# Kernel tuning notes

Hardware: AMD Instinct MI355X
Metric: run time of the kernel (lower is better)

## Reference

```python
import jax, jax.numpy as jnp
import numpy as np
import math

N = 30000
E = 600000
IN_DIM = 256
HID = 64
EMB = 64
HEADS = 4
EPS = 1e-5


def _glorot(key, shape):
    fan_in, fan_out = shape[0], shape[1]
    lim = math.sqrt(6.0 / (fan_in + fan_out))
    return jax.random.uniform(key, shape, jnp.float32, -lim, lim)


def setup_inputs() -> dict:
    key = jax.random.key(0)
    ks = jax.random.split(key, 24)
    inp = {
        "x": jax.random.normal(ks[0], (N, IN_DIM), jnp.float32),
        "edge_index": jax.random.randint(ks[1], (2, E), 0, N, jnp.int64),
    }
    # layer 1: in=IN_DIM, out per head=HID, heads=HEADS -> width HID*HEADS
    w1 = HID * HEADS
    inp.update({
        "w1q": _glorot(ks[2], (IN_DIM, w1)), "b1q": jnp.zeros((w1,), jnp.float32),
        "w1k": _glorot(ks[3], (IN_DIM, w1)), "b1k": jnp.zeros((w1,), jnp.float32),
        "w1v": _glorot(ks[4], (IN_DIM, w1)), "b1v": jnp.zeros((w1,), jnp.float32),
        "w1s": _glorot(ks[5], (IN_DIM, w1)), "b1s": jnp.zeros((w1,), jnp.float32),
        "g1": jnp.ones((w1,), jnp.float32), "be1": jnp.zeros((w1,), jnp.float32),
    })
    # layer 2: in=HID*HEADS, out per head=EMB -> width EMB*HEADS
    w2 = EMB * HEADS
    inp.update({
        "w2q": _glorot(ks[6], (w1, w2)), "b2q": jnp.zeros((w2,), jnp.float32),
        "w2k": _glorot(ks[7], (w1, w2)), "b2k": jnp.zeros((w2,), jnp.float32),
        "w2v": _glorot(ks[8], (w1, w2)), "b2v": jnp.zeros((w2,), jnp.float32),
        "w2s": _glorot(ks[9], (w1, w2)), "b2s": jnp.zeros((w2,), jnp.float32),
        "g2": jnp.ones((w2,), jnp.float32), "be2": jnp.zeros((w2,), jnp.float32),
    })
    return inp


def transformer_conv(x, edge_index, wq, bq, wk, bk, wv, bv, ws, bs, heads, out_ch):
    n = x.shape[0]
    q = (x @ wq + bq).reshape(n, heads, out_ch)
    k = (x @ wk + bk).reshape(n, heads, out_ch)
    v = (x @ wv + bv).reshape(n, heads, out_ch)
    src, dst = edge_index[0], edge_index[1]
    # per-edge gather: [E, H, C]
    qi, kj, vj = q[dst], k[src], v[src]
    alpha = jnp.sum(qi * kj, axis=-1) / math.sqrt(out_ch)  # [E, H]
    # segment softmax over incoming edges of each target node
    amax = jax.lax.stop_gradient(jax.ops.segment_max(alpha, dst, num_segments=n))
    ex = jnp.exp(alpha - amax[dst])
    denom = jax.ops.segment_sum(ex, dst, num_segments=n)
    alpha = ex / denom[dst]
    # scatter-add weighted values back to targets
    out = jax.ops.segment_sum(vj * alpha[..., None], dst, num_segments=n)
    out = out.reshape(n, heads * out_ch)
    return out + x @ ws + bs  # root/skip connection


def batch_norm(x, gamma, beta):
    mean = jnp.mean(x, axis=0)
    var = jnp.mean(jnp.square(x - mean), axis=0)  # biased, training-mode BN
    return (x - mean) * jax.lax.rsqrt(var + EPS) * gamma + beta


def leaky_relu(x):
    return jnp.where(x >= 0, x, 0.1 * x)


def reference(x, edge_index, w1q, b1q, w1k, b1k, w1v, b1v, w1s, b1s, g1, be1,
              w2q, b2q, w2k, b2k, w2v, b2v, w2s, b2s, g2, be2):
    h = transformer_conv(x, edge_index, w1q, b1q, w1k, b1k, w1v, b1v, w1s, b1s, HEADS, HID)
    h = leaky_relu(batch_norm(h, g1, be1))
    h = transformer_conv(h, edge_index, w2q, b2q, w2k, b2k, w2v, b2v, w2s, b2s, HEADS, EMB)
    h = leaky_relu(batch_norm(h, g2, be2))
    return h
```

## Files before the change

### kernel.cpp

```cpp
#include <hip/hip_runtime.h>
#include <math.h>

#define NODES 30000
#define EDGES 600000
#define QKVS_W 1024
#define OUT_W 256
#define BN_EPS 1e-5f

typedef _Float16 f16x8 __attribute__((ext_vector_type(8)));
typedef _Float16 half2t __attribute__((ext_vector_type(2)));
typedef __attribute__((ext_vector_type(4))) float f32x4;

__device__ __forceinline__ unsigned short f2h(float f) {
    union { _Float16 h; unsigned short u; } v;
    v.h = (_Float16)f;
    return v.u;
}
__device__ __forceinline__ float h2f(unsigned short u) {
    union { unsigned short u; _Float16 h; } v; v.u = u;
    return (float)v.h;
}
__device__ __forceinline__ half2t u2h2(unsigned int u) {
    union { unsigned int u; half2t h; } v; v.u = u;
    return v.h;
}

__device__ __forceinline__ float fdot2(half2t a, half2t b, float c) {
#if __has_builtin(__builtin_amdgcn_fdot2)
    return __builtin_amdgcn_fdot2(a, b, c, false);
#else
    return fmaf((float)a.x, (float)b.x, fmaf((float)a.y, (float)b.y, c));
#endif
}

template<int CTRL>
__device__ __forceinline__ float dpp_xor_add(float x) {
    int xi = __builtin_bit_cast(int, x);
    int yi = __builtin_amdgcn_mov_dpp(xi, CTRL, 0xF, 0xF, true);
    return x + __builtin_bit_cast(float, yi);
}

typedef const __attribute__((address_space(1))) void* gas_p;
typedef __attribute__((address_space(3))) void* las_p;
__device__ __forceinline__ void gload_lds16(const void* g, void* l) {
    __builtin_amdgcn_global_load_lds((gas_p)g, (las_p)l, 16, 0, 0);
}


__global__ __launch_bounds__(256) void k_count(const int* __restrict__ ei, int* __restrict__ deg) {
    int e = blockIdx.x * 256 + threadIdx.x;
    if (e < EDGES) atomicAdd(&deg[ei[EDGES + e]], 1);
}

__global__ __launch_bounds__(256) void k_blocksum(const int* __restrict__ deg, int* __restrict__ bsum) {
    __shared__ int sh[256];
    int i = blockIdx.x * 256 + threadIdx.x;
    sh[threadIdx.x] = (i < NODES) ? deg[i] : 0;
    __syncthreads();
    for (int off = 128; off > 0; off >>= 1) {
        if (threadIdx.x < off) sh[threadIdx.x] += sh[threadIdx.x + off];
        __syncthreads();
    }
    if (threadIdx.x == 0) bsum[blockIdx.x] = sh[0];
}

__global__ __launch_bounds__(128) void k_scanb(const int* __restrict__ bsum, int* __restrict__ bbase, int nb) {
    __shared__ int sh[128];
    int t = threadIdx.x;
    int v = (t < nb) ? bsum[t] : 0;
    sh[t] = v;
    __syncthreads();
    for (int off = 1; off < 128; off <<= 1) {
        int add = (t >= off) ? sh[t - off] : 0;
        __syncthreads();
        sh[t] += add;
        __syncthreads();
    }
    if (t < nb) bbase[t] = sh[t] - v;
}

__global__ __launch_bounds__(256) void k_localscan(const int* __restrict__ deg, const int* __restrict__ bbase,
                                                   int* __restrict__ rowptr, int* __restrict__ cursor) {
    __shared__ int sh[256];
    int i = blockIdx.x * 256 + threadIdx.x;
    int v = (i < NODES) ? deg[i] : 0;
    sh[threadIdx.x] = v;
    __syncthreads();
    for (int off = 1; off < 256; off <<= 1) {
        int add = (threadIdx.x >= off) ? sh[threadIdx.x - off] : 0;
        __syncthreads();
        sh[threadIdx.x] += add;
        __syncthreads();
    }
    if (i < NODES) {
        int p = bbase[blockIdx.x] + sh[threadIdx.x] - v;
        rowptr[i] = p;
        cursor[i] = p;
    }
}

__global__ __launch_bounds__(256) void k_fill(const int* __restrict__ ei, int* __restrict__ cursor,
                                              int* __restrict__ csr_src) {
    int e = blockIdx.x * 256 + threadIdx.x;
    if (e < EDGES) {
        int s = ei[e];
        int d = ei[EDGES + e];
        int slot = atomicAdd(&cursor[d], 1);
        csr_src[slot] = s;
    }
}


__global__ __launch_bounds__(256) void k_castA(const float* __restrict__ in, unsigned short* __restrict__ out, int n8) {
    int i = blockIdx.x * 256 + threadIdx.x;
    if (i >= n8) return;
    const float4* p = (const float4*)(in + (size_t)i * 8);
    float4 v0 = p[0], v1 = p[1];
    ushort4 o0, o1;
    o0.x = f2h(v0.x); o0.y = f2h(v0.y); o0.z = f2h(v0.z); o0.w = f2h(v0.w);
    o1.x = f2h(v1.x); o1.y = f2h(v1.y); o1.z = f2h(v1.z); o1.w = f2h(v1.w);
    ushort4* q = (ushort4*)(out + (size_t)i * 8);
    q[0] = o0; q[1] = o1;
}

__global__ __launch_bounds__(256) void k_castW2(
    const float* __restrict__ Wa0, const float* __restrict__ Wa1,
    const float* __restrict__ Wa2, const float* __restrict__ Wa3,
    const float* __restrict__ Ba0, const float* __restrict__ Ba1,
    const float* __restrict__ Ba2, const float* __restrict__ Ba3,
    const float* __restrict__ Wb0, const float* __restrict__ Wb1,
    const float* __restrict__ Wb2, const float* __restrict__ Wb3,
    const float* __restrict__ Bb0, const float* __restrict__ Bb1,
    const float* __restrict__ Bb2, const float* __restrict__ Bb3,
    unsigned short* __restrict__ Wt1, float* __restrict__ bf1,
    unsigned short* __restrict__ Wt2, float* __restrict__ bf2)
{
    int nn0 = blockIdx.x;
    int layer = nn0 >> 10;
    int n = nn0 & 1023;
    int k = threadIdx.x;
    int wsel = n >> 8, nc = n & 255;
    const float* W; const float* Bv;
    if (layer == 0) {
        W  = (wsel == 0) ? Wa0 : (wsel == 1) ? Wa1 : (wsel == 2) ? Wa2 : Wa3;
        Bv = (wsel == 0) ? Ba0 : (wsel == 1) ? Ba1 : (wsel == 2) ? Ba2 : Ba3;
    } else {
        W  = (wsel == 0) ? Wb0 : (wsel == 1) ? Wb1 : (wsel == 2) ? Wb2 : Wb3;
        Bv = (wsel == 0) ? Bb0 : (wsel == 1) ? Bb1 : (wsel == 2) ? Bb2 : Bb3;
    }
    unsigned short* Wt = (layer == 0) ? Wt1 : Wt2;
    float* bfused = (layer == 0) ? bf1 : bf2;
    Wt[(size_t)n * 256 + k] = f2h(W[(size_t)k * 256 + nc]);
    if (k == 0) bfused[n] = Bv[nc];
}


#define CS 136

__global__ __launch_bounds__(256) void k_gemm_f16(
    const unsigned short* __restrict__ A,
    const unsigned short* __restrict__ Wt,
    const float* __restrict__ bias,
    unsigned short* __restrict__ C, int M)
{
    __shared__ unsigned short sbuf[128 * CS];
    unsigned short* As = sbuf;
    unsigned short* Bs = sbuf + 8192;
    int tid = threadIdx.x;
    int lane = tid & 63;
    int wave = tid >> 6;
    int wm = wave & 1, wn = wave >> 1;
    int row0 = blockIdx.x * 128;
    int n0 = blockIdx.y * 128;

    f32x4 acc[4][4] = {};

    for (int k0 = 0; k0 < 256; k0 += 64) {
        #pragma unroll
        for (int w = 0; w < 4; w++) {
            int c = w * 256 + tid;
            int row = c >> 3;
            int cole = (c & 7) * 8;
            int ar = row0 + row; if (ar >= M) ar = M - 1;
            gload_lds16(&A[(size_t)ar * 256 + k0 + cole], &As[w * 2048 + tid * 8]);
            gload_lds16(&Wt[(size_t)(n0 + row) * 256 + k0 + cole], &Bs[w * 2048 + tid * 8]);
        }
        __syncthreads();
        int rsel = lane & 15;
        int kq = (lane >> 4) * 8;
        #pragma unroll
        for (int kh = 0; kh < 2; kh++) {
            f16x8 af[4], bfr[4];
            #pragma unroll
            for (int t = 0; t < 4; t++) {
                af[t]  = *reinterpret_cast<const f16x8*>(&As[(wm * 64 + t * 16 + rsel) * 64 + kh * 32 + kq]);
                bfr[t] = *reinterpret_cast<const f16x8*>(&Bs[(wn * 64 + t * 16 + rsel) * 64 + kh * 32 + kq]);
            }
            #pragma unroll
            for (int mt = 0; mt < 4; mt++)
                #pragma unroll
                for (int nt = 0; nt < 4; nt++)
                    acc[mt][nt] = __builtin_amdgcn_mfma_f32_16x16x32_f16(af[mt], bfr[nt], acc[mt][nt], 0, 0, 0);
        }
        __syncthreads();
    }

    int crow = (lane >> 4) * 4;
    int ccol = lane & 15;
    #pragma unroll
    for (int mt = 0; mt < 4; mt++) {
        int lrow = wm * 64 + mt * 16 + crow;
        #pragma unroll
        for (int nt = 0; nt < 4; nt++) {
            int lcol = wn * 64 + nt * 16 + ccol;
            float bv = bias[n0 + lcol];
            #pragma unroll
            for (int r = 0; r < 4; r++)
                sbuf[(lrow + r) * CS + lcol] = f2h(acc[mt][nt][r] + bv);
        }
    }
    __syncthreads();
    int chunk = tid & 15;
    int rbase = tid >> 4;
    #pragma unroll
    for (int g = 0; g < 8; g++) {
        int row_l = g * 16 + rbase;
        int gr = row0 + row_l;
        if (gr < M) {
            uint4 val = *(const uint4*)&sbuf[row_l * CS + chunk * 8];
            *(uint4*)&C[(size_t)gr * QKVS_W + n0 + chunk * 8] = val;
        }
    }
}


__global__ __launch_bounds__(256) void k_attn_f16(const unsigned short* __restrict__ qkvs,
                                                  const int* __restrict__ rowptr,
                                                  const int* __restrict__ deg,
                                                  const int* __restrict__ csr_src,
                                                  float* __restrict__ out)
{
    int wave = threadIdx.x >> 6;
    int lane = threadIdx.x & 63;
    int node = blockIdx.x * 4 + wave;
    if (node >= NODES) return;
    int half = lane >> 5;
    int lh = lane & 31;

    const unsigned short* qrow = qkvs + (size_t)node * QKVS_W;
    uint4 qv = *(const uint4*)&qrow[lh * 8];

    int start = rowptr[node];
    int cnt = deg[node];

    float m = -INFINITY, L = 0.f;
    float acc[8] = {0.f, 0.f, 0.f, 0.f, 0.f, 0.f, 0.f, 0.f};

    if (cnt > 0) {
        int clast = cnt - 1;
        #define CPOS(p) (start + (((2 * (p) + half) > clast) ? clast : (2 * (p) + half)))
        int i0  = csr_src[CPOS(0)];
        int i1  = csr_src[CPOS(1)];
        int ixA = csr_src[CPOS(2)];
        int ixB = csr_src[CPOS(3)];
        uint4 kA, vA, kB, vB;
        {
            const unsigned short* p = qkvs + (size_t)i0 * QKVS_W + lh * 8;
            kA = *(const uint4*)(p + 256);
            vA = *(const uint4*)(p + 512);
        }
        {
            const unsigned short* p = qkvs + (size_t)i1 * QKVS_W + lh * 8;
            kB = *(const uint4*)(p + 256);
            vB = *(const uint4*)(p + 512);
        }
        int npairs = (cnt + 1) >> 1;
        for (int i = 0; i < npairs; i += 2) {
            {
                const unsigned short* pA = qkvs + (size_t)ixA * QKVS_W + lh * 8;
                ixA = csr_src[CPOS(i + 4)];
                float d  = fdot2(u2h2(qv.x), u2h2(kA.x), 0.f);
                d        = fdot2(u2h2(qv.y), u2h2(kA.y), d);
                float d2 = fdot2(u2h2(qv.z), u2h2(kA.z), 0.f);
                d2       = fdot2(u2h2(qv.w), u2h2(kA.w), d2);
                d += d2;
                kA = *(const uint4*)(pA + 256);
                d = dpp_xor_add<0xB1>(d);
                d = dpp_xor_add<0x4E>(d);
                d = dpp_xor_add<0x141>(d);
                float al = d * 0.125f;
                bool valid = (2 * i + half) < cnt;
                if (valid) {
                    if (__any(al > m + 8.f)) {
                        float nm = fmaxf(m, al);
                        float sc = __expf(m - nm);
                        L *= sc;
                        #pragma unroll
                        for (int t = 0; t < 8; t++) acc[t] *= sc;
                        m = nm;
                    }
                    float p = __expf(al - m);
                    L += p;
                    half2t vh0 = u2h2(vA.x), vh1 = u2h2(vA.y);
                    half2t vh2 = u2h2(vA.z), vh3 = u2h2(vA.w);
                    acc[0] = fmaf((float)vh0.x, p, acc[0]);
                    acc[1] = fmaf((float)vh0.y, p, acc[1]);
                    acc[2] = fmaf((float)vh1.x, p, acc[2]);
                    acc[3] = fmaf((float)vh1.y, p, acc[3]);
                    acc[4] = fmaf((float)vh2.x, p, acc[4]);
                    acc[5] = fmaf((float)vh2.y, p, acc[5]);
                    acc[6] = fmaf((float)vh3.x, p, acc[6]);
                    acc[7] = fmaf((float)vh3.y, p, acc[7]);
                }
                vA = *(const uint4*)(pA + 512);
            }
            {
                const unsigned short* pB = qkvs + (size_t)ixB * QKVS_W + lh * 8;
                ixB = csr_src[CPOS(i + 5)];
                float d  = fdot2(u2h2(qv.x), u2h2(kB.x), 0.f);
                d        = fdot2(u2h2(qv.y), u2h2(kB.y), d);
                float d2 = fdot2(u2h2(qv.z), u2h2(kB.z), 0.f);
                d2       = fdot2(u2h2(qv.w), u2h2(kB.w), d2);
                d += d2;
                kB = *(const uint4*)(pB + 256);
                d = dpp_xor_add<0xB1>(d);
                d = dpp_xor_add<0x4E>(d);
                d = dpp_xor_add<0x141>(d);
                float al = d * 0.125f;
                bool valid = (2 * (i + 1) + half) < cnt;
                if (valid) {
                    if (__any(al > m + 8.f)) {
                        float nm = fmaxf(m, al);
                        float sc = __expf(m - nm);
                        L *= sc;
                        #pragma unroll
                        for (int t = 0; t < 8; t++) acc[t] *= sc;
                        m = nm;
                    }
                    float p = __expf(al - m);
                    L += p;
                    half2t vh0 = u2h2(vB.x), vh1 = u2h2(vB.y);
                    half2t vh2 = u2h2(vB.z), vh3 = u2h2(vB.w);
                    acc[0] = fmaf((float)vh0.x, p, acc[0]);
                    acc[1] = fmaf((float)vh0.y, p, acc[1]);
                    acc[2] = fmaf((float)vh1.x, p, acc[2]);
                    acc[3] = fmaf((float)vh1.y, p, acc[3]);
                    acc[4] = fmaf((float)vh2.x, p, acc[4]);
                    acc[5] = fmaf((float)vh2.y, p, acc[5]);
                    acc[6] = fmaf((float)vh3.x, p, acc[6]);
                    acc[7] = fmaf((float)vh3.y, p, acc[7]);
                }
                vB = *(const uint4*)(pB + 512);
            }
        }
        #undef CPOS
    }

    float mo = __shfl_xor(m, 32, 64);
    float Lo = __shfl_xor(L, 32, 64);
    float nm = fmaxf(m, mo);
    float scs = (L  > 0.f) ? __expf(m  - nm) : 0.f;
    float sco = (Lo > 0.f) ? __expf(mo - nm) : 0.f;
    float Lt = fmaf(L, scs, Lo * sco);
    float inv = (Lt > 0.f) ? 1.f / Lt : 0.f;
    float t0 = fmaf(acc[0], scs, __shfl_xor(acc[0], 32, 64) * sco);
    float t1 = fmaf(acc[1], scs, __shfl_xor(acc[1], 32, 64) * sco);
    float t2 = fmaf(acc[2], scs, __shfl_xor(acc[2], 32, 64) * sco);
    float t3 = fmaf(acc[3], scs, __shfl_xor(acc[3], 32, 64) * sco);
    float t4 = fmaf(acc[4], scs, __shfl_xor(acc[4], 32, 64) * sco);
    float t5 = fmaf(acc[5], scs, __shfl_xor(acc[5], 32, 64) * sco);
    float t6 = fmaf(acc[6], scs, __shfl_xor(acc[6], 32, 64) * sco);
    float t7 = fmaf(acc[7], scs, __shfl_xor(acc[7], 32, 64) * sco);
    float w0 = half ? t4 : t0;
    float w1 = half ? t5 : t1;
    float w2 = half ? t6 : t2;
    float w3 = half ? t7 : t3;
    ushort4 sv = *(const ushort4*)&qrow[768 + lh * 8 + half * 4];
    float4 o;
    o.x = fmaf(w0, inv, h2f(sv.x));
    o.y = fmaf(w1, inv, h2f(sv.y));
    o.z = fmaf(w2, inv, h2f(sv.z));
    o.w = fmaf(w3, inv, h2f(sv.w));
    *(float4*)&out[(size_t)node * OUT_W + lh * 8 + half * 4] = o;
}


__global__ __launch_bounds__(256) void k_bnstats(const float* __restrict__ h,
                                                 float* __restrict__ sum, float* __restrict__ sumsq) {
    int col = threadIdx.x;
    int r0 = blockIdx.x * 64;
    int r1 = min(r0 + 64, NODES);
    float s = 0.f, s2 = 0.f;
    for (int r = r0; r < r1; r++) {
        float v = h[(size_t)r * OUT_W + col];
        s += v; s2 += v * v;
    }
    atomicAdd(&sum[col], s);
    atomicAdd(&sumsq[col], s2);
}

__device__ __forceinline__ float4 bn_scale4(const float* sum, const float* sumsq,
                                            const float* g, const float* be,
                                            int col, float4* shift) {
    float4 s  = *(const float4*)&sum[col];
    float4 s2 = *(const float4*)&sumsq[col];
    float4 gv = *(const float4*)&g[col];
    float4 bv = *(const float4*)&be[col];
    const float invN = 1.0f / NODES;
    float4 sc, sh;
    float mean, var;
    mean = s.x * invN; var = fmaxf(s2.x * invN - mean * mean, 0.f);
    sc.x = gv.x * rsqrtf(var + BN_EPS); sh.x = bv.x - mean * sc.x;
    mean = s.y * invN; var = fmaxf(s2.y * invN - mean * mean, 0.f);
    sc.y = gv.y * rsqrtf(var + BN_EPS); sh.y = bv.y - mean * sc.y;
    mean = s.z * invN; var = fmaxf(s2.z * invN - mean * mean, 0.f);
    sc.z = gv.z * rsqrtf(var + BN_EPS); sh.z = bv.z - mean * sc.z;
    mean = s.w * invN; var = fmaxf(s2.w * invN - mean * mean, 0.f);
    sc.w = gv.w * rsqrtf(var + BN_EPS); sh.w = bv.w - mean * sc.w;
    *shift = sh;
    return sc;
}

__global__ __launch_bounds__(256) void k_bnapply_f16(const float* __restrict__ h,
                                                     const float* __restrict__ sum,
                                                     const float* __restrict__ sumsq,
                                                     const float* __restrict__ g,
                                                     const float* __restrict__ be,
                                                     unsigned short* __restrict__ out) {
    int idx = blockIdx.x * 256 + threadIdx.x;
    int base = idx * 4;
    int col = base & (OUT_W - 1);
    float4 sh;
    float4 sc = bn_scale4(sum, sumsq, g, be, col, &sh);
    float4 v = *(const float4*)&h[base];
    float4 o;
    o.x = v.x * sc.x + sh.x; o.x = (o.x >= 0.f) ? o.x : 0.1f * o.x;
    o.y = v.y * sc.y + sh.y; o.y = (o.y >= 0.f) ? o.y : 0.1f * o.y;
    o.z = v.z * sc.z + sh.z; o.z = (o.z >= 0.f) ? o.z : 0.1f * o.z;
    o.w = v.w * sc.w + sh.w; o.w = (o.w >= 0.f) ? o.w : 0.1f * o.w;
    ushort4 u; u.x = f2h(o.x); u.y = f2h(o.y); u.z = f2h(o.z); u.w = f2h(o.w);
    *(ushort4*)&out[base] = u;
}

__global__ __launch_bounds__(256) void k_bnapply(const float* __restrict__ h,
                                                 const float* __restrict__ sum,
                                                 const float* __restrict__ sumsq,
                                                 const float* __restrict__ g,
                                                 const float* __restrict__ be,
                                                 float* __restrict__ out) {
    int idx = blockIdx.x * 256 + threadIdx.x;
    int base = idx * 4;
    int col = base & (OUT_W - 1);
    float4 sh;
    float4 sc = bn_scale4(sum, sumsq, g, be, col, &sh);
    float4 v = *(const float4*)&h[base];
    float4 o;
    o.x = v.x * sc.x + sh.x; o.x = (o.x >= 0.f) ? o.x : 0.1f * o.x;
    o.y = v.y * sc.y + sh.y; o.y = (o.y >= 0.f) ? o.y : 0.1f * o.y;
    o.z = v.z * sc.z + sh.z; o.z = (o.z >= 0.f) ? o.z : 0.1f * o.z;
    o.w = v.w * sc.w + sh.w; o.w = (o.w >= 0.f) ? o.w : 0.1f * o.w;
    *(float4*)&out[base] = o;
}


extern "C" void kernel_launch(void* const* d_in, const int* in_sizes, int n_in,
                              void* d_out, int out_size, void* d_ws, size_t ws_size,
                              hipStream_t stream) {
    const float* x  = (const float*)d_in[0];
    const int*   ei = (const int*)d_in[1];
    const float* w1[4] = {(const float*)d_in[2], (const float*)d_in[4], (const float*)d_in[6], (const float*)d_in[8]};
    const float* b1[4] = {(const float*)d_in[3], (const float*)d_in[5], (const float*)d_in[7], (const float*)d_in[9]};
    const float* g1  = (const float*)d_in[10];
    const float* be1 = (const float*)d_in[11];
    const float* w2[4] = {(const float*)d_in[12], (const float*)d_in[14], (const float*)d_in[16], (const float*)d_in[18]};
    const float* b2[4] = {(const float*)d_in[13], (const float*)d_in[15], (const float*)d_in[17], (const float*)d_in[19]};
    const float* g2  = (const float*)d_in[20];
    const float* be2 = (const float*)d_in[21];

    char* ws = (char*)d_ws;
    unsigned short* qkvsb  = (unsigned short*)(ws);
    float*          h1     = (float*)(ws + 61440000);
    unsigned short* abuf   = (unsigned short*)(ws + 92160000);
    unsigned short* wt1    = (unsigned short*)(ws + 107520000);
    unsigned short* wt2    = (unsigned short*)(ws + 108044288);
    float*          b1f    = (float*)(ws + 108568576);
    float*          b2f    = (float*)(ws + 108572672);
    int*            deg    = (int*)  (ws + 108576768);
    int*            rowptr = (int*)  (ws + 108696768);
    int*            cursor = (int*)  (ws + 108816768);
    int*            csr    = (int*)  (ws + 108936768);
    int*            bsum   = (int*)  (ws + 111336768);
    int*            bbase  = (int*)  (ws + 111337280);
    float*          sum1   = (float*)(ws + 111337792);
    float*          sq1    = (float*)(ws + 111338816);
    float*          sum2   = (float*)(ws + 111339840);
    float*          sq2    = (float*)(ws + 111340864);

    hipMemsetAsync(deg, 0, NODES * sizeof(int), stream);
    hipMemsetAsync(sum1, 0, 4096, stream);

    const int EB = (EDGES + 255) / 256;
    const int NB = (NODES + 255) / 256;

    k_castA<<<(NODES * 256 / 8 + 255) / 256, 256, 0, stream>>>(x, abuf, NODES * 256 / 8);
    k_castW2<<<2048, 256, 0, stream>>>(w1[0], w1[1], w1[2], w1[3], b1[0], b1[1], b1[2], b1[3],
                                       w2[0], w2[1], w2[2], w2[3], b2[0], b2[1], b2[2], b2[3],
                                       wt1, b1f, wt2, b2f);

    k_count    <<<EB, 256, 0, stream>>>(ei, deg);
    k_blocksum <<<NB, 256, 0, stream>>>(deg, bsum);
    k_scanb    <<<1, 128, 0, stream>>>(bsum, bbase, NB);
    k_localscan<<<NB, 256, 0, stream>>>(deg, bbase, rowptr, cursor);
    k_fill     <<<EB, 256, 0, stream>>>(ei, cursor, csr);

    dim3 ggrid((NODES + 127) / 128, 8);
    const int ANB = NODES / 4;
    const int APB = (NODES * OUT_W / 4) / 256;
    const int SNB = (NODES + 63) / 64;

    k_gemm_f16   <<<ggrid, 256, 0, stream>>>(abuf, wt1, b1f, qkvsb, NODES);
    k_attn_f16   <<<ANB, 256, 0, stream>>>(qkvsb, rowptr, deg, csr, h1);
    k_bnstats    <<<SNB, 256, 0, stream>>>(h1, sum1, sq1);
    k_bnapply_f16<<<APB, 256, 0, stream>>>(h1, sum1, sq1, g1, be1, abuf);

    k_gemm_f16   <<<ggrid, 256, 0, stream>>>(abuf, wt2, b2f, qkvsb, NODES);
    k_attn_f16   <<<ANB, 256, 0, stream>>>(qkvsb, rowptr, deg, csr, h1);
    k_bnstats    <<<SNB, 256, 0, stream>>>(h1, sum2, sq2);
    k_bnapply    <<<APB, 256, 0, stream>>>(h1, sum2, sq2, g2, be2, (float*)d_out);
}
```

Measured before the change: 510.8 us.

## Split QKVS buffer into separate Q/S, K fp16, and FP8 V arrays

The GEMM epilogue now writes Q and skip into one 512-wide fp16 buffer, K into its own dense 256-wide fp16 buffer, and V as FP8 (e4m3) into a 256-byte-per-row buffer. The attention kernel gathers K and V from these compact arrays and decodes V with the packed fp8-to-f32 conversion. This cuts the bytes moved by the random per-edge gathers and packs the gathered rows more tightly for better cache use. The cost is lower V precision, which may push results outside tolerance, plus extra encode and decode work.

```diff
diff --git a/kernel.cpp b/kernel.cpp
--- a/kernel.cpp
+++ b/kernel.cpp
@@ -3,12 +3,15 @@
 
 #define NODES 30000
 #define EDGES 600000
-#define QKVS_W 1024
+#define QS_W 512
+#define K_W 256
+#define KV_W 256
 #define OUT_W 256
 #define BN_EPS 1e-5f
 
 typedef _Float16 f16x8 __attribute__((ext_vector_type(8)));
 typedef _Float16 half2t __attribute__((ext_vector_type(2)));
+typedef float f32x2 __attribute__((ext_vector_type(2)));
 typedef __attribute__((ext_vector_type(4))) float f32x4;
 
 __device__ __forceinline__ unsigned short f2h(float f) {
@@ -31,6 +34,54 @@
 #else
     return fmaf((float)a.x, (float)b.x, fmaf((float)a.y, (float)b.y, c));
 #endif
+}
+
+
+__device__ __forceinline__ void dec8(uint2 w, float* f) {
+#if __has_builtin(__builtin_amdgcn_cvt_pk_f32_fp8)
+    f32x2 a = __builtin_amdgcn_cvt_pk_f32_fp8((int)w.x, false);
+    f32x2 b = __builtin_amdgcn_cvt_pk_f32_fp8((int)w.x, true);
+    f32x2 c = __builtin_amdgcn_cvt_pk_f32_fp8((int)w.y, false);
+    f32x2 d = __builtin_amdgcn_cvt_pk_f32_fp8((int)w.y, true);
+    f[0] = a.x; f[1] = a.y; f[2] = b.x; f[3] = b.y;
+    f[4] = c.x; f[5] = c.y; f[6] = d.x; f[7] = d.y;
+#else
+    #pragma unroll
+    for (int j = 0; j < 8; j++) {
+        unsigned int byte = ((j < 4 ? w.x : w.y) >> ((j & 3) * 8)) & 0xFF;
+        unsigned short h = (unsigned short)(((byte & 0x80u) << 8) | ((byte & 0x7Fu) << 7));
+        f[j] = h2f(h) * 256.0f;
+    }
+#endif
+}
+
+__device__ __forceinline__ uint2 enc8(uint4 w) {
+    float f[8];
+    f[0] = h2f((unsigned short)(w.x & 0xffff)); f[1] = h2f((unsigned short)(w.x >> 16));
+    f[2] = h2f((unsigned short)(w.y & 0xffff)); f[3] = h2f((unsigned short)(w.y >> 16));
+    f[4] = h2f((unsigned short)(w.z & 0xffff)); f[5] = h2f((unsigned short)(w.z >> 16));
+    f[6] = h2f((unsigned short)(w.w & 0xffff)); f[7] = h2f((unsigned short)(w.w >> 16));
+    uint2 r;
+#if __has_builtin(__builtin_amdgcn_cvt_pk_fp8_f32)
+    int lo = 0, hi = 0;
+    lo = __builtin_amdgcn_cvt_pk_fp8_f32(f[0], f[1], lo, false);
+    lo = __builtin_amdgcn_cvt_pk_fp8_f32(f[2], f[3], lo, true);
+    hi = __builtin_amdgcn_cvt_pk_fp8_f32(f[4], f[5], hi, false);
+    hi = __builtin_amdgcn_cvt_pk_fp8_f32(f[6], f[7], hi, true);
+    r.x = (unsigned)lo; r.y = (unsigned)hi;
+#else
+    unsigned b[8];
+    #pragma unroll
+    for (int j = 0; j < 8; j++) {
+        unsigned short hb = f2h(f[j] * 0.00390625f);
+        unsigned m = hb & 0x7fffu;
+        unsigned rr = m + 0x3Fu + ((m >> 7) & 1u);
+        b[j] = ((hb >> 8) & 0x80u) | ((rr >> 7) & 0x7Fu);
+    }
+    r.x = b[0] | (b[1] << 8) | (b[2] << 16) | (b[3] << 24);
+    r.y = b[4] | (b[5] << 8) | (b[6] << 16) | (b[7] << 24);
+#endif
+    return r;
 }
 
 template<int CTRL>
@@ -161,7 +212,9 @@
     const unsigned short* __restrict__ A,
     const unsigned short* __restrict__ Wt,
     const float* __restrict__ bias,
-    unsigned short* __restrict__ C, int M)
+    unsigned short* __restrict__ QS,
+    unsigned short* __restrict__ K16,
+    unsigned char* __restrict__ V8, int M)
 {
     __shared__ unsigned short sbuf[128 * CS];
     unsigned short* As = sbuf;
@@ -222,19 +275,47 @@
     __syncthreads();
     int chunk = tid & 15;
     int rbase = tid >> 4;
-    #pragma unroll
-    for (int g = 0; g < 8; g++) {
-        int row_l = g * 16 + rbase;
-        int gr = row0 + row_l;
-        if (gr < M) {
-            uint4 val = *(const uint4*)&sbuf[row_l * CS + chunk * 8];
-            *(uint4*)&C[(size_t)gr * QKVS_W + n0 + chunk * 8] = val;
-        }
-    }
-}
-
-
-__global__ __launch_bounds__(256) void k_attn_f16(const unsigned short* __restrict__ qkvs,
+    if (n0 < 256 || n0 >= 768) {
+        int cbase = (n0 < 256) ? n0 : (n0 - 512);
+        #pragma unroll
+        for (int g = 0; g < 8; g++) {
+            int row_l = g * 16 + rbase;
+            int gr = row0 + row_l;
+            if (gr < M) {
+                uint4 val = *(const uint4*)&sbuf[row_l * CS + chunk * 8];
+                *(uint4*)&QS[(size_t)gr * QS_W + cbase + chunk * 8] = val;
+            }
+        }
+    } else if (n0 < 512) {
+        int cbase = n0 - 256;
+        #pragma unroll
+        for (int g = 0; g < 8; g++) {
+            int row_l = g * 16 + rbase;
+            int gr = row0 + row_l;
+            if (gr < M) {
+                uint4 val = *(const uint4*)&sbuf[row_l * CS + chunk * 8];
+                *(uint4*)&K16[(size_t)gr * K_W + cbase + chunk * 8] = val;
+            }
+        }
+    } else {
+        int cbase = n0 - 512;
+        #pragma unroll
+        for (int g = 0; g < 8; g++) {
+            int row_l = g * 16 + rbase;
+            int gr = row0 + row_l;
+            if (gr < M) {
+                uint4 val = *(const uint4*)&sbuf[row_l * CS + chunk * 8];
+                uint2 enc = enc8(val);
+                *(uint2*)&V8[(size_t)gr * KV_W + cbase + chunk * 8] = enc;
+            }
+        }
+    }
+}
+
+
+__global__ __launch_bounds__(256) void k_attn_mix(const unsigned short* __restrict__ qs,
+                                                  const unsigned short* __restrict__ k16,
+                                                  const unsigned char* __restrict__ v8,
                                                   const int* __restrict__ rowptr,
                                                   const int* __restrict__ deg,
                                                   const int* __restrict__ csr_src,
@@ -247,7 +328,7 @@
     int half = lane >> 5;
     int lh = lane & 31;
 
-    const unsigned short* qrow = qkvs + (size_t)node * QKVS_W;
+    const unsigned short* qrow = qs + (size_t)node * QS_W;
     uint4 qv = *(const uint4*)&qrow[lh * 8];
 
     int start = rowptr[node];
@@ -263,28 +344,24 @@
         int i1  = csr_src[CPOS(1)];
         int ixA = csr_src[CPOS(2)];
         int ixB = csr_src[CPOS(3)];
-        uint4 kA, vA, kB, vB;
-        {
-            const unsigned short* p = qkvs + (size_t)i0 * QKVS_W + lh * 8;
-            kA = *(const uint4*)(p + 256);
-            vA = *(const uint4*)(p + 512);
-        }
-        {
-            const unsigned short* p = qkvs + (size_t)i1 * QKVS_W + lh * 8;
-            kB = *(const uint4*)(p + 256);
-            vB = *(const uint4*)(p + 512);
-        }
+        uint4 kA, kB;
+        uint2 vA, vB;
+        kA = *(const uint4*)&k16[(size_t)i0 * K_W + lh * 8];
+        vA = *(const uint2*)&v8[(size_t)i0 * KV_W + lh * 8];
+        kB = *(const uint4*)&k16[(size_t)i1 * K_W + lh * 8];
+        vB = *(const uint2*)&v8[(size_t)i1 * KV_W + lh * 8];
         int npairs = (cnt + 1) >> 1;
         for (int i = 0; i < npairs; i += 2) {
             {
-                const unsigned short* pA = qkvs + (size_t)ixA * QKVS_W + lh * 8;
+                const unsigned short* pkA = k16 + (size_t)ixA * K_W + lh * 8;
+                const unsigned char*  pvA = v8  + (size_t)ixA * KV_W + lh * 8;
                 ixA = csr_src[CPOS(i + 4)];
                 float d  = fdot2(u2h2(qv.x), u2h2(kA.x), 0.f);
                 d        = fdot2(u2h2(qv.y), u2h2(kA.y), d);
                 float d2 = fdot2(u2h2(qv.z), u2h2(kA.z), 0.f);
                 d2       = fdot2(u2h2(qv.w), u2h2(kA.w), d2);
                 d += d2;
-                kA = *(const uint4*)(pA + 256);
+                kA = *(const uint4*)pkA;
                 d = dpp_xor_add<0xB1>(d);
                 d = dpp_xor_add<0x4E>(d);
                 d = dpp_xor_add<0x141>(d);
@@ -301,28 +378,23 @@
                     }
                     float p = __expf(al - m);
                     L += p;
-                    half2t vh0 = u2h2(vA.x), vh1 = u2h2(vA.y);
-                    half2t vh2 = u2h2(vA.z), vh3 = u2h2(vA.w);
-                    acc[0] = fmaf((float)vh0.x, p, acc[0]);
-                    acc[1] = fmaf((float)vh0.y, p, acc[1]);
-                    acc[2] = fmaf((float)vh1.x, p, acc[2]);
-                    acc[3] = fmaf((float)vh1.y, p, acc[3]);
-                    acc[4] = fmaf((float)vh2.x, p, acc[4]);
-                    acc[5] = fmaf((float)vh2.y, p, acc[5]);
-                    acc[6] = fmaf((float)vh3.x, p, acc[6]);
-                    acc[7] = fmaf((float)vh3.y, p, acc[7]);
+                    float vf[8];
+                    dec8(vA, vf);
+                    #pragma unroll
+                    for (int t = 0; t < 8; t++) acc[t] = fmaf(p, vf[t], acc[t]);
                 }
-                vA = *(const uint4*)(pA + 512);
+                vA = *(const uint2*)pvA;
             }
             {
-                const unsigned short* pB = qkvs + (size_t)ixB * QKVS_W + lh * 8;
+                const unsigned short* pkB = k16 + (size_t)ixB * K_W + lh * 8;
+                const unsigned char*  pvB = v8  + (size_t)ixB * KV_W + lh * 8;
                 ixB = csr_src[CPOS(i + 5)];
                 float d  = fdot2(u2h2(qv.x), u2h2(kB.x), 0.f);
                 d        = fdot2(u2h2(qv.y), u2h2(kB.y), d);
                 float d2 = fdot2(u2h2(qv.z), u2h2(kB.z), 0.f);
                 d2       = fdot2(u2h2(qv.w), u2h2(kB.w), d2);
                 d += d2;
-                kB = *(const uint4*)(pB + 256);
+                kB = *(const uint4*)pkB;
                 d = dpp_xor_add<0xB1>(d);
                 d = dpp_xor_add<0x4E>(d);
                 d = dpp_xor_add<0x141>(d);
@@ -339,18 +411,12 @@
                     }
                     float p = __expf(al - m);
                     L += p;
-                    half2t vh0 = u2h2(vB.x), vh1 = u2h2(vB.y);
-                    half2t vh2 = u2h2(vB.z), vh3 = u2h2(vB.w);
-                    acc[0] = fmaf((float)vh0.x, p, acc[0]);
-                    acc[1] = fmaf((float)vh0.y, p, acc[1]);
-                    acc[2] = fmaf((float)vh1.x, p, acc[2]);
-                    acc[3] = fmaf((float)vh1.y, p, acc[3]);
-                    acc[4] = fmaf((float)vh2.x, p, acc[4]);
-                    acc[5] = fmaf((float)vh2.y, p, acc[5]);
-                    acc[6] = fmaf((float)vh3.x, p, acc[6]);
-                    acc[7] = fmaf((float)vh3.y, p, acc[7]);
+                    float vf[8];
+                    dec8(vB, vf);
+                    #pragma unroll
+                    for (int t = 0; t < 8; t++) acc[t] = fmaf(p, vf[t], acc[t]);
                 }
-                vB = *(const uint4*)(pB + 512);
+                vB = *(const uint2*)pvB;
             }
         }
         #undef CPOS
@@ -375,7 +441,7 @@
     float w1 = half ? t5 : t1;
     float w2 = half ? t6 : t2;
     float w3 = half ? t7 : t3;
-    ushort4 sv = *(const ushort4*)&qrow[768 + lh * 8 + half * 4];
+    ushort4 sv = *(const ushort4*)&qrow[256 + lh * 8 + half * 4];
     float4 o;
     o.x = fmaf(w0, inv, h2f(sv.x));
     o.y = fmaf(w1, inv, h2f(sv.y));
@@ -478,23 +544,25 @@
     const float* be2 = (const float*)d_in[21];
 
     char* ws = (char*)d_ws;
-    unsigned short* qkvsb  = (unsigned short*)(ws);
-    float*          h1     = (float*)(ws + 61440000);
-    unsigned short* abuf   = (unsigned short*)(ws + 92160000);
-    unsigned short* wt1    = (unsigned short*)(ws + 107520000);
-    unsigned short* wt2    = (unsigned short*)(ws + 108044288);
-    float*          b1f    = (float*)(ws + 108568576);
-    float*          b2f    = (float*)(ws + 108572672);
-    int*            deg    = (int*)  (ws + 108576768);
-    int*            rowptr = (int*)  (ws + 108696768);
-    int*            cursor = (int*)  (ws + 108816768);
-    int*            csr    = (int*)  (ws + 108936768);
-    int*            bsum   = (int*)  (ws + 111336768);
-    int*            bbase  = (int*)  (ws + 111337280);
-    float*          sum1   = (float*)(ws + 111337792);
-    float*          sq1    = (float*)(ws + 111338816);
-    float*          sum2   = (float*)(ws + 111339840);
-    float*          sq2    = (float*)(ws + 111340864);
+    unsigned short* qsb    = (unsigned short*)(ws);
+    unsigned short* k16b   = (unsigned short*)(ws + 30720000);
+    unsigned char*  v8b    = (unsigned char*)(ws + 46080000);
+    float*          h1     = (float*)(ws + 53760000);
+    unsigned short* abuf   = (unsigned short*)(ws + 84480000);
+    unsigned short* wt1    = (unsigned short*)(ws + 99840000);
+    unsigned short* wt2    = (unsigned short*)(ws + 100364288);
+    float*          b1f    = (float*)(ws + 100888576);
+    float*          b2f    = (float*)(ws + 100892672);
+    int*            deg    = (int*)  (ws + 100896768);
+    int*            rowptr = (int*)  (ws + 101016768);
+    int*            cursor = (int*)  (ws + 101136768);
+    int*            csr    = (int*)  (ws + 101256768);
+    int*            bsum   = (int*)  (ws + 103656768);
+    int*            bbase  = (int*)  (ws + 103657280);
+    float*          sum1   = (float*)(ws + 103657792);
+    float*          sq1    = (float*)(ws + 103658816);
+    float*          sum2   = (float*)(ws + 103659840);
+    float*          sq2    = (float*)(ws + 103660864);
 
     hipMemsetAsync(deg, 0, NODES * sizeof(int), stream);
     hipMemsetAsync(sum1, 0, 4096, stream);
@@ -518,13 +586,13 @@
     const int APB = (NODES * OUT_W / 4) / 256;
     const int SNB = (NODES + 63) / 64;
 
-    k_gemm_f16   <<<ggrid, 256, 0, stream>>>(abuf, wt1, b1f, qkvsb, NODES);
-    k_attn_f16   <<<ANB, 256, 0, stream>>>(qkvsb, rowptr, deg, csr, h1);
+    k_gemm_f16   <<<ggrid, 256, 0, stream>>>(abuf, wt1, b1f, qsb, k16b, v8b, NODES);
+    k_attn_mix   <<<ANB, 256, 0, stream>>>(qsb, k16b, v8b, rowptr, deg, csr, h1);
     k_bnstats    <<<SNB, 256, 0, stream>>>(h1, sum1, sq1);
     k_bnapply_f16<<<APB, 256, 0, stream>>>(h1, sum1, sq1, g1, be1, abuf);
 
-    k_gemm_f16   <<<ggrid, 256, 0, stream>>>(abuf, wt2, b2f, qkvsb, NODES);
-    k_attn_f16   <<<ANB, 256, 0, stream>>>(qkvsb, rowptr, deg, csr, h1);
+    k_gemm_f16   <<<ggrid, 256, 0, stream>>>(abuf, wt2, b2f, qsb, k16b, v8b, NODES);
+    k_attn_mix   <<<ANB, 256, 0, stream>>>(qsb, k16b, v8b, rowptr, deg, csr, h1);
     k_bnstats    <<<SNB, 256, 0, stream>>>(h1, sum2, sq2);
     k_bnapply    <<<APB, 256, 0, stream>>>(h1, sum2, sq2, g2, be2, (float*)d_out);
 }
```

Result: faster. 470.5 us (-7.9%).
